# Kernel tuning notes

Hardware: AMD Instinct MI355X
Metric: run time of the kernel (lower is better)

## Reference

```python
import jax, jax.numpy as jnp
import numpy as np
from jax import lax

NEG_SLOPE = 0.01
UP = 2
DN = 2
FILTER_LEN = 8

def kaiser_filter(n, fc, beta):
    # Kaiser-windowed sinc lowpass, unit DC gain (standard StyleGAN3-style design)
    t = np.arange(n) - (n - 1) / 2.0
    f = 2.0 * fc * np.sinc(2.0 * fc * t) * np.kaiser(n, beta)
    f = f / f.sum()
    return jnp.asarray(f, dtype=jnp.float32)

def _depthwise_conv1d(x, filt, stride, lhs_dilation, pad_lo, pad_hi):
    # x: [B, C, T]; filt: [K] symmetric taps -> depthwise kernel [C, 1, K]
    C = x.shape[1]
    w = jnp.broadcast_to(filt.reshape(1, 1, -1), (C, 1, filt.shape[0]))
    return lax.conv_general_dilated(
        x, w,
        window_strides=(stride,),
        padding=[(pad_lo, pad_hi)],
        lhs_dilation=(lhs_dilation,),
        dimension_numbers=("NCW", "OIW", "NCW"),
        feature_group_count=C,
    )

def setup_inputs() -> dict:
    key = jax.random.key(0)
    x = jax.random.normal(key, (8, 256, 32768), dtype=jnp.float32)
    up_filter = kaiser_filter(FILTER_LEN * UP + 1, 0.5, 2.5)   # 17 taps
    dn_filter = kaiser_filter(FILTER_LEN * DN + 1, 0.5, 2.5)   # 17 taps
    return {"x": x, "up_filter": up_filter, "dn_filter": dn_filter}

def reference(x, up_filter, dn_filter):
    B, C, T = x.shape
    K = up_filter.shape[0]  # UP*FILTER_LEN + 1
    # conv_transpose1d(stride=UP, padding=p, output_padding=UP-1) ==
    # conv with lhs_dilation=UP and padding (K-1-p, K-1-p+output_padding).
    # Filter is symmetric so kernel flip is a no-op.
    p = UP * FILTER_LEN // 2
    y = _depthwise_conv1d(x, up_filter, stride=1, lhs_dilation=UP,
                          pad_lo=K - 1 - p, pad_hi=K - 1 - p + (UP - 1))
    y = UP * y  # [B, C, UP*T]
    y = jnp.where(y >= 0, y, NEG_SLOPE * y)  # leaky_relu
    pd = DN * FILTER_LEN // 2
    y = _depthwise_conv1d(y, dn_filter, stride=DN, lhs_dilation=1,
                          pad_lo=pd, pad_hi=pd)  # [B, C, T]
    return y
```

## Files before the change

kernel.cpp:

```cpp
#include <hip/hip_runtime.h>
#include <stdint.h>


#define T_LEN 32768
#define R_OUT 8

typedef __fp16   cvt2 __attribute__((ext_vector_type(2)));
typedef _Float16 hpair __attribute__((ext_vector_type(2)));

__device__ __forceinline__ uint32_t pkrtz(float lo, float hi) {
    cvt2 p = __builtin_amdgcn_cvt_pkrtz(lo, hi);
    return __builtin_bit_cast(uint32_t, p);
}
__device__ __forceinline__ hpair h2(uint32_t u) {
    return __builtin_bit_cast(hpair, u);
}
__device__ __forceinline__ uint32_t u32(hpair h) {
    return __builtin_bit_cast(uint32_t, h);
}
__device__ __forceinline__ hpair pk_fma(hpair a, hpair b, hpair c) {
    return __builtin_elementwise_fma(a, b, c);
}
__device__ __forceinline__ hpair pk_lrelu(hpair v, hpair c01) {
    return __builtin_elementwise_max(v, v * c01);
}

__global__ void pack_taps(const float* __restrict__ up,
                          const float* __restrict__ dn,
                          uint32_t* __restrict__ ws) {
    if (threadIdx.x == 0 && blockIdx.x == 0) {
        #pragma unroll
        for (int j = 0; j < 9; ++j) {
            float fe = 2.0f * up[2*j];
            float de = dn[2*j];
            ws[j]      = pkrtz(fe, fe);
            ws[17 + j] = pkrtz(de, de);
        }
        #pragma unroll
        for (int j = 0; j < 8; ++j) {
            float fo = 2.0f * up[2*j+1];
            float dd = dn[2*j+1];
            ws[9 + j]  = pkrtz(fo, fo);
            ws[26 + j] = pkrtz(dd, dd);
        }
    }
}

__device__ __forceinline__ void pairs4(
    const float* xv, const hpair* feB, const hpair* foB, hpair c01,
    uint32_t* ga, uint32_t* go)
{
    uint32_t xau[8], xsu[7];
    #pragma unroll
    for (int k = 0; k < 8; ++k) xau[k] = pkrtz(xv[2*k], xv[2*k+1]);
    #pragma unroll
    for (int k = 0; k < 7; ++k)
        xsu[k] = (xau[k] >> 16) | (xau[k+1] << 16);

    #pragma unroll
    for (int q = 0; q < 4; ++q) {
        hpair s = feB[0] * h2(xau[q]);
        #pragma unroll
        for (int a = 1; a < 5; ++a) s = pk_fma(feB[2*a], h2(xau[q+a]), s);
        #pragma unroll
        for (int a = 0; a < 4; ++a) s = pk_fma(feB[2*a+1], h2(xsu[q+a]), s);
        ga[q] = u32(pk_lrelu(s, c01));

        hpair r = foB[0] * h2(xsu[q]);
        #pragma unroll
        for (int a = 1; a < 4; ++a) r = pk_fma(foB[2*a], h2(xsu[q+a]), r);
        #pragma unroll
        for (int a = 0; a < 4; ++a) r = pk_fma(foB[2*a+1], h2(xau[q+a+1]), r);
        go[q] = u32(pk_lrelu(r, c01));
    }
}

__global__ void flrelu_wshare(
    const float* __restrict__ x,
    const uint32_t* __restrict__ tw,
    float* __restrict__ out)
{
    __shared__ __align__(16) uint32_t sga[4][66][4];
    __shared__ __align__(16) uint32_t sgb[4][66][4];

    const int tid  = threadIdx.x;
    const int lane = tid & 63;
    const int wv   = tid >> 6;
    const int gid  = blockIdx.x * 256 + tid;
    const int row  = gid >> 12;
    const int t    = (gid & 4095) * R_OUT;
    const float* __restrict__ xrow = x + (size_t)row * T_LEN;
    float* __restrict__ orow       = out + (size_t)row * T_LEN;

    hpair feB[9], foB[8], deB[9], ddB[8];
    #pragma unroll
    for (int j = 0; j < 9; ++j) { feB[j] = h2(tw[j]); deB[j] = h2(tw[17+j]); }
    #pragma unroll
    for (int j = 0; j < 8; ++j) { foB[j] = h2(tw[9+j]); ddB[j] = h2(tw[26+j]); }
    const hpair c01 = h2(pkrtz(0.01f, 0.01f));

    uint32_t ga[4], go[4];
    {
        float xv[16];
        if (t >= 8) {
            const float4* xp = reinterpret_cast<const float4*>(xrow + t - 8);
            float4 v0 = xp[0], v1 = xp[1], v2 = xp[2], v3 = xp[3];
            xv[0]=v0.x; xv[1]=v0.y; xv[2]=v0.z; xv[3]=v0.w;
            xv[4]=v1.x; xv[5]=v1.y; xv[6]=v1.z; xv[7]=v1.w;
            xv[8]=v2.x; xv[9]=v2.y; xv[10]=v2.z; xv[11]=v2.w;
            xv[12]=v3.x; xv[13]=v3.y; xv[14]=v3.z; xv[15]=v3.w;
        } else {
            #pragma unroll
            for (int i = 0; i < 16; ++i) {
                int g = t - 8 + i;
                xv[i] = (g >= 0) ? xrow[g] : 0.0f;
            }
        }
        pairs4(xv, feB, foB, c01, ga, go);
        if (t == 0) {
            ga[0] = 0u; go[0] = 0u; ga[1] = 0u; go[1] = 0u;
        }
        *reinterpret_cast<uint4*>(&sga[wv][lane][0]) =
            make_uint4(ga[0], ga[1], ga[2], ga[3]);
        *reinterpret_cast<uint4*>(&sgb[wv][lane][0]) =
            make_uint4(go[0], go[1], go[2], go[3]);
    }

    if (lane == 63) {
        const int tx = t + R_OUT;
        float xv[16];
        if (tx + 7 < T_LEN) {
            const float4* xp = reinterpret_cast<const float4*>(xrow + tx - 8);
            float4 v0 = xp[0], v1 = xp[1], v2 = xp[2], v3 = xp[3];
            xv[0]=v0.x; xv[1]=v0.y; xv[2]=v0.z; xv[3]=v0.w;
            xv[4]=v1.x; xv[5]=v1.y; xv[6]=v1.z; xv[7]=v1.w;
            xv[8]=v2.x; xv[9]=v2.y; xv[10]=v2.z; xv[11]=v2.w;
            xv[12]=v3.x; xv[13]=v3.y; xv[14]=v3.z; xv[15]=v3.w;
        } else {
            #pragma unroll
            for (int i = 0; i < 16; ++i) {
                int g = tx - 8 + i;
                xv[i] = (g < T_LEN) ? xrow[g] : 0.0f;
            }
        }
        uint32_t ha[4], hb[4];
        pairs4(xv, feB, foB, c01, ha, hb);
        if (tx + 3 >= T_LEN) {
            #pragma unroll
            for (int q = 0; q < 4; ++q) {
                int m0 = tx - 4 + 2*q;
                uint32_t msk = ((m0   < T_LEN) ? 0x0000FFFFu : 0u)
                             | ((m0+1 < T_LEN) ? 0xFFFF0000u : 0u);
                ha[q] &= msk; hb[q] &= msk;
            }
        }
        *reinterpret_cast<uint4*>(&sga[wv][64][0]) =
            make_uint4(ha[0], ha[1], ha[2], ha[3]);
        *reinterpret_cast<uint4*>(&sgb[wv][64][0]) =
            make_uint4(hb[0], hb[1], hb[2], hb[3]);
    }

    {
        uint4 GN = *reinterpret_cast<const uint4*>(&sga[wv][lane + 1][0]);
        uint4 ON = *reinterpret_cast<const uint4*>(&sgb[wv][lane + 1][0]);
        uint32_t gaF[8] = {ga[0], ga[1], ga[2], ga[3], GN.x, GN.y, GN.z, GN.w};
        uint32_t goF[8] = {go[0], go[1], go[2], go[3], ON.x, ON.y, ON.z, ON.w};

        uint32_t gs[7], gos[7];
        #pragma unroll
        for (int k = 0; k < 7; ++k) {
            gs[k]  = (gaF[k] >> 16) | (gaF[k+1] << 16);
            gos[k] = (goF[k] >> 16) | (goF[k+1] << 16);
        }

        hpair zp[4];
        #pragma unroll
        for (int p = 0; p < 4; ++p) {
            hpair s = deB[0] * h2(gaF[p]);
            #pragma unroll
            for (int a = 1; a < 5; ++a) s = pk_fma(deB[2*a], h2(gaF[p+a]), s);
            #pragma unroll
            for (int a = 0; a < 4; ++a) s = pk_fma(deB[2*a+1], h2(gs[p+a]), s);
            #pragma unroll
            for (int a = 0; a < 4; ++a) s = pk_fma(ddB[2*a], h2(goF[p+a]), s);
            #pragma unroll
            for (int a = 0; a < 4; ++a) s = pk_fma(ddB[2*a+1], h2(gos[p+a]), s);
            zp[p] = s;
        }

        float4* op = reinterpret_cast<float4*>(orow + t);
        op[0] = make_float4((float)zp[0][0], (float)zp[0][1],
                            (float)zp[1][0], (float)zp[1][1]);
        op[1] = make_float4((float)zp[2][0], (float)zp[2][1],
                            (float)zp[3][0], (float)zp[3][1]);
    }
}

extern "C" void kernel_launch(void* const* d_in, const int* in_sizes, int n_in,
                              void* d_out, int out_size, void* d_ws, size_t ws_size,
                              hipStream_t stream) {
    const float* x  = (const float*)d_in[0];
    const float* up = (const float*)d_in[1];
    const float* dn = (const float*)d_in[2];
    float* out      = (float*)d_out;
    uint32_t* ws    = (uint32_t*)d_ws;

    pack_taps<<<1, 64, 0, stream>>>(up, dn, ws);

    const int rows    = in_sizes[0] / T_LEN;
    const int threads = rows * (T_LEN / R_OUT);
    flrelu_wshare<<<threads / 256, 256, 0, stream>>>(x, ws, out);
}
```

Measured before the change: 108.8 us.

## Process two half-row tiles per thread with loads issued up front

```diff
diff --git a/kernel.cpp b/kernel.cpp
--- a/kernel.cpp
+++ b/kernel.cpp
@@ -4,6 +4,7 @@
 
 #define T_LEN 32768
 #define R_OUT 8
+#define HALF  16384
 
 typedef __fp16   cvt2 __attribute__((ext_vector_type(2)));
 typedef _Float16 hpair __attribute__((ext_vector_type(2)));
@@ -75,20 +76,106 @@
     }
 }
 
-__global__ void flrelu_wshare(
+#define PROCESS_TILE(TI, XV, TT)                                             \
+{                                                                            \
+    uint32_t ga[4], go[4];                                                   \
+    pairs4(XV, feB, foB, c01, ga, go);                                       \
+    if ((TT) == 0) { ga[0]=0u; go[0]=0u; ga[1]=0u; go[1]=0u; }               \
+    *reinterpret_cast<uint4*>(&sga[TI][wv][lane][0]) =                       \
+        make_uint4(ga[0], ga[1], ga[2], ga[3]);                              \
+    *reinterpret_cast<uint4*>(&sgb[TI][wv][lane][0]) =                       \
+        make_uint4(go[0], go[1], go[2], go[3]);                              \
+    if (lane >= 60) {                                                        \
+        const int q  = lane - 60;                                            \
+        const int tx = ((TT) - lane * R_OUT) + 512;                          \
+        float xw[12];                                                        \
+        if (tx + 2*q + 3 < T_LEN) {                                          \
+            const float2* xp2 =                                              \
+                reinterpret_cast<const float2*>(xrow + tx - 8 + 2*q);        \
+            _Pragma("unroll")                                                \
+            for (int k = 0; k < 6; ++k) {                                    \
+                float2 v = xp2[k];                                           \
+                xw[2*k] = v.x; xw[2*k+1] = v.y;                              \
+            }                                                                \
+        } else {                                                             \
+            _Pragma("unroll")                                                \
+            for (int i = 0; i < 12; ++i) {                                   \
+                int g = tx - 8 + 2*q + i;                                    \
+                xw[i] = (g < T_LEN) ? xrow[g] : 0.0f;                        \
+            }                                                                \
+        }                                                                    \
+        uint32_t hau[5], hsu[4];                                             \
+        _Pragma("unroll")                                                    \
+        for (int k = 0; k < 5; ++k) hau[k] = pkrtz(xw[2*k], xw[2*k+1]);      \
+        _Pragma("unroll")                                                    \
+        for (int k = 0; k < 4; ++k)                                          \
+            hsu[k] = (hau[k] >> 16) | (hau[k+1] << 16);                      \
+        hpair s = feB[0] * h2(hau[0]);                                       \
+        _Pragma("unroll")                                                    \
+        for (int a = 1; a < 5; ++a) s = pk_fma(feB[2*a], h2(hau[a]), s);     \
+        _Pragma("unroll")                                                    \
+        for (int a = 0; a < 4; ++a) s = pk_fma(feB[2*a+1], h2(hsu[a]), s);   \
+        uint32_t ha = u32(pk_lrelu(s, c01));                                 \
+        hpair r = foB[0] * h2(hsu[0]);                                       \
+        _Pragma("unroll")                                                    \
+        for (int a = 1; a < 4; ++a) r = pk_fma(foB[2*a], h2(hsu[a]), r);     \
+        _Pragma("unroll")                                                    \
+        for (int a = 0; a < 4; ++a) r = pk_fma(foB[2*a+1], h2(hau[a+1]), r); \
+        uint32_t hb = u32(pk_lrelu(r, c01));                                 \
+        const int m0 = tx - 4 + 2*q;                                         \
+        const uint32_t msk = ((m0   < T_LEN) ? 0x0000FFFFu : 0u)             \
+                           | ((m0+1 < T_LEN) ? 0xFFFF0000u : 0u);            \
+        sga[TI][wv][64][q] = ha & msk;                                       \
+        sgb[TI][wv][64][q] = hb & msk;                                       \
+    }                                                                        \
+    __builtin_amdgcn_wave_barrier();         \
+    {                                                                        \
+        uint4 GN = *reinterpret_cast<const uint4*>(&sga[TI][wv][lane+1][0]); \
+        uint4 ON = *reinterpret_cast<const uint4*>(&sgb[TI][wv][lane+1][0]); \
+        uint32_t gaF[8] = {ga[0],ga[1],ga[2],ga[3],GN.x,GN.y,GN.z,GN.w};     \
+        uint32_t goF[8] = {go[0],go[1],go[2],go[3],ON.x,ON.y,ON.z,ON.w};     \
+        uint32_t gsh[7], gosh[7];                                            \
+        _Pragma("unroll")                                                    \
+        for (int k = 0; k < 7; ++k) {                                        \
+            gsh[k]  = (gaF[k] >> 16) | (gaF[k+1] << 16);                     \
+            gosh[k] = (goF[k] >> 16) | (goF[k+1] << 16);                     \
+        }                                                                    \
+        hpair zp[4];                                                         \
+        _Pragma("unroll")                                                    \
+        for (int p = 0; p < 4; ++p) {                                        \
+            hpair s = deB[0] * h2(gaF[p]);                                   \
+            _Pragma("unroll")                                                \
+            for (int a = 1; a < 5; ++a) s = pk_fma(deB[2*a], h2(gaF[p+a]), s); \
+            _Pragma("unroll")                                                \
+            for (int a = 0; a < 4; ++a) s = pk_fma(deB[2*a+1], h2(gsh[p+a]), s); \
+            _Pragma("unroll")                                                \
+            for (int a = 0; a < 4; ++a) s = pk_fma(ddB[2*a], h2(goF[p+a]), s); \
+            _Pragma("unroll")                                                \
+            for (int a = 0; a < 4; ++a) s = pk_fma(ddB[2*a+1], h2(gosh[p+a]), s); \
+            zp[p] = s;                                                       \
+        }                                                                    \
+        float4* op = reinterpret_cast<float4*>(orow + (TT));                 \
+        op[0] = make_float4((float)zp[0][0], (float)zp[0][1],                \
+                            (float)zp[1][0], (float)zp[1][1]);               \
+        op[1] = make_float4((float)zp[2][0], (float)zp[2][1],                \
+                            (float)zp[3][0], (float)zp[3][1]);               \
+    }                                                                        \
+}
+
+__global__ void flrelu_pf2b(
     const float* __restrict__ x,
     const uint32_t* __restrict__ tw,
     float* __restrict__ out)
 {
-    __shared__ __align__(16) uint32_t sga[4][66][4];
-    __shared__ __align__(16) uint32_t sgb[4][66][4];
+    __shared__ __align__(16) uint32_t sga[2][4][66][4];
+    __shared__ __align__(16) uint32_t sgb[2][4][66][4];
 
     const int tid  = threadIdx.x;
     const int lane = tid & 63;
     const int wv   = tid >> 6;
     const int gid  = blockIdx.x * 256 + tid;
-    const int row  = gid >> 12;
-    const int t    = (gid & 4095) * R_OUT;
+    const int row  = gid >> 11;
+    const int t    = (gid & 2047) * R_OUT;
     const float* __restrict__ xrow = x + (size_t)row * T_LEN;
     float* __restrict__ orow       = out + (size_t)row * T_LEN;
 
@@ -99,101 +186,36 @@
     for (int j = 0; j < 8; ++j) { foB[j] = h2(tw[9+j]); ddB[j] = h2(tw[26+j]); }
     const hpair c01 = h2(pkrtz(0.01f, 0.01f));
 
-    uint32_t ga[4], go[4];
+    float xvA[16], xvB[16];
+    if (t >= 8) {
+        const float4* xp = reinterpret_cast<const float4*>(xrow + t - 8);
+        float4 v0 = xp[0], v1 = xp[1], v2 = xp[2], v3 = xp[3];
+        xvA[0]=v0.x; xvA[1]=v0.y; xvA[2]=v0.z; xvA[3]=v0.w;
+        xvA[4]=v1.x; xvA[5]=v1.y; xvA[6]=v1.z; xvA[7]=v1.w;
+        xvA[8]=v2.x; xvA[9]=v2.y; xvA[10]=v2.z; xvA[11]=v2.w;
+        xvA[12]=v3.x; xvA[13]=v3.y; xvA[14]=v3.z; xvA[15]=v3.w;
+    } else {
+        #pragma unroll
+        for (int i = 0; i < 16; ++i) {
+            int g = t - 8 + i;
+            xvA[i] = (g >= 0) ? xrow[g] : 0.0f;
+        }
+    }
     {
-        float xv[16];
-        if (t >= 8) {
-            const float4* xp = reinterpret_cast<const float4*>(xrow + t - 8);
-            float4 v0 = xp[0], v1 = xp[1], v2 = xp[2], v3 = xp[3];
-            xv[0]=v0.x; xv[1]=v0.y; xv[2]=v0.z; xv[3]=v0.w;
-            xv[4]=v1.x; xv[5]=v1.y; xv[6]=v1.z; xv[7]=v1.w;
-            xv[8]=v2.x; xv[9]=v2.y; xv[10]=v2.z; xv[11]=v2.w;
-            xv[12]=v3.x; xv[13]=v3.y; xv[14]=v3.z; xv[15]=v3.w;
-        } else {
-            #pragma unroll
-            for (int i = 0; i < 16; ++i) {
-                int g = t - 8 + i;
-                xv[i] = (g >= 0) ? xrow[g] : 0.0f;
-            }
-        }
-        pairs4(xv, feB, foB, c01, ga, go);
-        if (t == 0) {
-            ga[0] = 0u; go[0] = 0u; ga[1] = 0u; go[1] = 0u;
-        }
-        *reinterpret_cast<uint4*>(&sga[wv][lane][0]) =
-            make_uint4(ga[0], ga[1], ga[2], ga[3]);
-        *reinterpret_cast<uint4*>(&sgb[wv][lane][0]) =
-            make_uint4(go[0], go[1], go[2], go[3]);
-    }
-
-    if (lane == 63) {
-        const int tx = t + R_OUT;
-        float xv[16];
-        if (tx + 7 < T_LEN) {
-            const float4* xp = reinterpret_cast<const float4*>(xrow + tx - 8);
-            float4 v0 = xp[0], v1 = xp[1], v2 = xp[2], v3 = xp[3];
-            xv[0]=v0.x; xv[1]=v0.y; xv[2]=v0.z; xv[3]=v0.w;
-            xv[4]=v1.x; xv[5]=v1.y; xv[6]=v1.z; xv[7]=v1.w;
-            xv[8]=v2.x; xv[9]=v2.y; xv[10]=v2.z; xv[11]=v2.w;
-            xv[12]=v3.x; xv[13]=v3.y; xv[14]=v3.z; xv[15]=v3.w;
-        } else {
-            #pragma unroll
-            for (int i = 0; i < 16; ++i) {
-                int g = tx - 8 + i;
-                xv[i] = (g < T_LEN) ? xrow[g] : 0.0f;
-            }
-        }
-        uint32_t ha[4], hb[4];
-        pairs4(xv, feB, foB, c01, ha, hb);
-        if (tx + 3 >= T_LEN) {
-            #pragma unroll
-            for (int q = 0; q < 4; ++q) {
-                int m0 = tx - 4 + 2*q;
-                uint32_t msk = ((m0   < T_LEN) ? 0x0000FFFFu : 0u)
-                             | ((m0+1 < T_LEN) ? 0xFFFF0000u : 0u);
-                ha[q] &= msk; hb[q] &= msk;
-            }
-        }
-        *reinterpret_cast<uint4*>(&sga[wv][64][0]) =
-            make_uint4(ha[0], ha[1], ha[2], ha[3]);
-        *reinterpret_cast<uint4*>(&sgb[wv][64][0]) =
-            make_uint4(hb[0], hb[1], hb[2], hb[3]);
-    }
-
-    {
-        uint4 GN = *reinterpret_cast<const uint4*>(&sga[wv][lane + 1][0]);
-        uint4 ON = *reinterpret_cast<const uint4*>(&sgb[wv][lane + 1][0]);
-        uint32_t gaF[8] = {ga[0], ga[1], ga[2], ga[3], GN.x, GN.y, GN.z, GN.w};
-        uint32_t goF[8] = {go[0], go[1], go[2], go[3], ON.x, ON.y, ON.z, ON.w};
-
-        uint32_t gs[7], gos[7];
-        #pragma unroll
-        for (int k = 0; k < 7; ++k) {
-            gs[k]  = (gaF[k] >> 16) | (gaF[k+1] << 16);
-            gos[k] = (goF[k] >> 16) | (goF[k+1] << 16);
-        }
-
-        hpair zp[4];
-        #pragma unroll
-        for (int p = 0; p < 4; ++p) {
-            hpair s = deB[0] * h2(gaF[p]);
-            #pragma unroll
-            for (int a = 1; a < 5; ++a) s = pk_fma(deB[2*a], h2(gaF[p+a]), s);
-            #pragma unroll
-            for (int a = 0; a < 4; ++a) s = pk_fma(deB[2*a+1], h2(gs[p+a]), s);
-            #pragma unroll
-            for (int a = 0; a < 4; ++a) s = pk_fma(ddB[2*a], h2(goF[p+a]), s);
-            #pragma unroll
-            for (int a = 0; a < 4; ++a) s = pk_fma(ddB[2*a+1], h2(gos[p+a]), s);
-            zp[p] = s;
-        }
-
-        float4* op = reinterpret_cast<float4*>(orow + t);
-        op[0] = make_float4((float)zp[0][0], (float)zp[0][1],
-                            (float)zp[1][0], (float)zp[1][1]);
-        op[1] = make_float4((float)zp[2][0], (float)zp[2][1],
-                            (float)zp[3][0], (float)zp[3][1]);
-    }
+        const float4* xp = reinterpret_cast<const float4*>(xrow + t + HALF - 8);
+        float4 v0 = xp[0], v1 = xp[1], v2 = xp[2], v3 = xp[3];
+        xvB[0]=v0.x; xvB[1]=v0.y; xvB[2]=v0.z; xvB[3]=v0.w;
+        xvB[4]=v1.x; xvB[5]=v1.y; xvB[6]=v1.z; xvB[7]=v1.w;
+        xvB[8]=v2.x; xvB[9]=v2.y; xvB[10]=v2.z; xvB[11]=v2.w;
+        xvB[12]=v3.x; xvB[13]=v3.y; xvB[14]=v3.z; xvB[15]=v3.w;
+    }
+    #pragma unroll
+    for (int i = 0; i < 16; ++i) {
+        asm volatile("" : "+v"(xvB[i]));
+    }
+
+    PROCESS_TILE(0, xvA, t)
+    PROCESS_TILE(1, xvB, t + HALF)
 }
 
 extern "C" void kernel_launch(void* const* d_in, const int* in_sizes, int n_in,
@@ -208,6 +230,6 @@
     pack_taps<<<1, 64, 0, stream>>>(up, dn, ws);
 
     const int rows    = in_sizes[0] / T_LEN;
-    const int threads = rows * (T_LEN / R_OUT);
-    flrelu_wshare<<<threads / 256, 256, 0, stream>>>(x, ws, out);
-}
+    const int threads = rows * (T_LEN / (2 * R_OUT));
+    flrelu_pf2b<<<threads / 256, 256, 0, stream>>>(x, ws, out);
+}
```

Measured after the change: 113.9 us. 1.05x slower.
